# Kernel tuning notes

Measured on AMD Instinct MI355X. Metric: run time of the kernel, lower is better.

The kernel has to match this reference:

```python
import jax, jax.numpy as jnp
import numpy as np

B = 16384            # batch
F = 26               # number of categorical fields (columns of x)
FIELD_DIM = 100000   # vocab per field
D = 64               # base_embedding_dim
BLOCK_FIELDS = [list(range(0, 8)), list(range(8, 16)), list(range(16, 26))]
BLOCK_DIMS = [64, 32, 16]   # block 0 == base dim -> identity projector


def setup_inputs() -> dict:
    key = jax.random.key(0)
    ks = jax.random.split(key, 8)
    x = jax.random.randint(ks[0], (B, F), 0, FIELD_DIM, dtype=jnp.int32)
    # per-block embedding tables: rows = sum of field_dims of the block's fields
    t0 = jax.random.normal(ks[1], (len(BLOCK_FIELDS[0]) * FIELD_DIM, BLOCK_DIMS[0]), jnp.float32) * 0.02
    t1 = jax.random.normal(ks[2], (len(BLOCK_FIELDS[1]) * FIELD_DIM, BLOCK_DIMS[1]), jnp.float32) * 0.02
    t2 = jax.random.normal(ks[3], (len(BLOCK_FIELDS[2]) * FIELD_DIM, BLOCK_DIMS[2]), jnp.float32) * 0.02
    # projectors for blocks whose dim != base dim (torch Linear: y = x @ W.T + b)
    W1 = jax.random.normal(ks[4], (D, BLOCK_DIMS[1]), jnp.float32) * 0.05
    b1 = jnp.zeros((D,), jnp.float32)
    W2 = jax.random.normal(ks[5], (D, BLOCK_DIMS[2]), jnp.float32) * 0.05
    b2 = jnp.zeros((D,), jnp.float32)
    return {"x": x, "t0": t0, "t1": t1, "t2": t2, "W1": W1, "b1": b1, "W2": W2, "b2": b2}


def reference(x, t0, t1, t2, W1, b1, W2, b2):
    tables = [t0, t1, t2]
    projs = [None, (W1, b1), (W2, b2)]
    out = jnp.zeros((x.shape[0], D), dtype=t0.dtype)
    for blk in range(len(BLOCK_FIELDS)):
        fields = np.asarray(BLOCK_FIELDS[blk])                 # static column routing
        offs = jnp.arange(len(fields), dtype=x.dtype) * FIELD_DIM  # per-field row offsets
        idx = x[:, fields] + offs[None, :]                     # [B, nb]
        emb = tables[blk][idx]                                 # gather -> [B, nb, d_blk]
        if projs[blk] is not None:
            W, b = projs[blk]
            emb = jnp.einsum('bnd,od->bno', emb, W) + b        # project to base dim
        out = out + emb.sum(axis=1)                            # segment-sum over block's fields
    return out
```

## Files before the change

### kernel.cpp

```cpp
#include <hip/hip_runtime.h>
#include <hip/hip_bf16.h>

#define BATCH 16384
#define NFIELDS 26
#define FIELD_DIM 100000
#define BASED 64


__global__ __launch_bounds__(256) void mixdim_embbag_kernel(
    const int* __restrict__ x,
    const float* __restrict__ t0,
    const float* __restrict__ t1,
    const float* __restrict__ t2,
    const float* __restrict__ W1,
    const float* __restrict__ b1,
    const float* __restrict__ W2,
    const float* __restrict__ b2,
    float* __restrict__ out)
{
    const int lane = threadIdx.x & 63;
    const int wave = threadIdx.x >> 6;
    const int row  = blockIdx.x * 4 + wave;
    if (row >= BATCH) return;

    float w1r[32];
    {
        const float4* W1v = (const float4*)(W1 + lane * 32);
        #pragma unroll
        for (int i = 0; i < 8; ++i) {
            float4 v = W1v[i];
            w1r[4*i+0] = v.x; w1r[4*i+1] = v.y; w1r[4*i+2] = v.z; w1r[4*i+3] = v.w;
        }
    }
    float w2r[16];
    {
        const float4* W2v = (const float4*)(W2 + lane * 16);
        #pragma unroll
        for (int i = 0; i < 4; ++i) {
            float4 v = W2v[i];
            w2r[4*i+0] = v.x; w2r[4*i+1] = v.y; w2r[4*i+2] = v.z; w2r[4*i+3] = v.w;
        }
    }

    int xi = 0;
    if (lane < NFIELDS) xi = x[row * NFIELDS + lane];

    float acc = 0.f;
    #pragma unroll
    for (int f = 0; f < 8; ++f) {
        const int r = __shfl(xi, f) + f * FIELD_DIM;
        acc += t0[r * 64 + lane];
    }

    float s1 = 0.f;
    {
        const int d1 = lane & 31;
        #pragma unroll
        for (int f = 0; f < 8; ++f) {
            const int r = __shfl(xi, 8 + f) + f * FIELD_DIM;
            s1 += t1[r * 32 + d1];
        }
    }
    #pragma unroll
    for (int k = 0; k < 32; ++k)
        acc += __shfl(s1, k) * w1r[k];

    float s2 = 0.f;
    {
        const int d2 = lane & 15;
        #pragma unroll
        for (int f = 0; f < 10; ++f) {
            const int r = __shfl(xi, 16 + f) + f * FIELD_DIM;
            s2 += t2[r * 16 + d2];
        }
    }
    #pragma unroll
    for (int k = 0; k < 16; ++k)
        acc += __shfl(s2, k) * w2r[k];

    acc += 8.0f * b1[lane] + 10.0f * b2[lane];

    out[row * 64 + lane] = acc;
}

extern "C" void kernel_launch(void* const* d_in, const int* in_sizes, int n_in,
                              void* d_out, int out_size, void* d_ws, size_t ws_size,
                              hipStream_t stream) {
    const int*   x  = (const int*)  d_in[0];
    const float* t0 = (const float*)d_in[1];
    const float* t1 = (const float*)d_in[2];
    const float* t2 = (const float*)d_in[3];
    const float* W1 = (const float*)d_in[4];
    const float* b1 = (const float*)d_in[5];
    const float* W2 = (const float*)d_in[6];
    const float* b2 = (const float*)d_in[7];
    float* out = (float*)d_out;

    dim3 grid(BATCH / 4);
    dim3 block(256);
    hipLaunchKernelGGL(mixdim_embbag_kernel, grid, block, 0, stream,
                       x, t0, t1, t2, W1, b1, W2, b2, out);
}
```

Measured before the change: 329.3 us.

## Process two batch rows per wave with nontemporal table gathers

```diff
diff --git a/kernel.cpp b/kernel.cpp
--- a/kernel.cpp
+++ b/kernel.cpp
@@ -7,7 +7,11 @@
 #define BASED 64
 
 
-__global__ __launch_bounds__(256) void mixdim_embbag_kernel(
+__device__ __forceinline__ float ntload(const float* p) {
+    return __builtin_nontemporal_load(p);
+}
+
+__global__ __launch_bounds__(256, 4) void mixdim_embbag_kernel(
     const int* __restrict__ x,
     const float* __restrict__ t0,
     const float* __restrict__ t1,
@@ -20,8 +24,7 @@
 {
     const int lane = threadIdx.x & 63;
     const int wave = threadIdx.x >> 6;
-    const int row  = blockIdx.x * 4 + wave;
-    if (row >= BATCH) return;
+    const int row0 = (blockIdx.x * 4 + wave) * 2;
 
     float w1r[32];
     {
@@ -43,44 +46,65 @@
     }
 
     int xi = 0;
-    if (lane < NFIELDS) xi = x[row * NFIELDS + lane];
+    {
+        const int l = lane & 31;
+        const int r = row0 + (lane >> 5);
+        if (l < NFIELDS) xi = x[r * NFIELDS + l];
+    }
 
-    float acc = 0.f;
+    float acc0 = 0.f, acc1 = 0.f;
+
     #pragma unroll
     for (int f = 0; f < 8; ++f) {
-        const int r = __shfl(xi, f) + f * FIELD_DIM;
-        acc += t0[r * 64 + lane];
+        const int i0 = __shfl(xi, f)      + f * FIELD_DIM;
+        const int i1 = __shfl(xi, 32 + f) + f * FIELD_DIM;
+        acc0 += ntload(t0 + i0 * 64 + lane);
+        acc1 += ntload(t0 + i1 * 64 + lane);
     }
 
-    float s1 = 0.f;
+    float s1_0 = 0.f, s1_1 = 0.f;
     {
         const int d1 = lane & 31;
         #pragma unroll
-        for (int f = 0; f < 8; ++f) {
-            const int r = __shfl(xi, 8 + f) + f * FIELD_DIM;
-            s1 += t1[r * 32 + d1];
+        for (int j = 0; j < 8; ++j) {
+            const int i0 = __shfl(xi, 8 + j)      + j * FIELD_DIM;
+            const int i1 = __shfl(xi, 32 + 8 + j) + j * FIELD_DIM;
+            s1_0 += ntload(t1 + i0 * 32 + d1);
+            s1_1 += ntload(t1 + i1 * 32 + d1);
         }
     }
-    #pragma unroll
-    for (int k = 0; k < 32; ++k)
-        acc += __shfl(s1, k) * w1r[k];
 
-    float s2 = 0.f;
+    float s2_0 = 0.f, s2_1 = 0.f;
     {
         const int d2 = lane & 15;
         #pragma unroll
-        for (int f = 0; f < 10; ++f) {
-            const int r = __shfl(xi, 16 + f) + f * FIELD_DIM;
-            s2 += t2[r * 16 + d2];
+        for (int j = 0; j < 10; ++j) {
+            const int i0 = __shfl(xi, 16 + j)      + j * FIELD_DIM;
+            const int i1 = __shfl(xi, 32 + 16 + j) + j * FIELD_DIM;
+            s2_0 += ntload(t2 + i0 * 16 + d2);
+            s2_1 += ntload(t2 + i1 * 16 + d2);
         }
     }
+
     #pragma unroll
-    for (int k = 0; k < 16; ++k)
-        acc += __shfl(s2, k) * w2r[k];
+    for (int k = 0; k < 32; ++k) {
+        const float w = w1r[k];
+        acc0 += __shfl(s1_0, k) * w;
+        acc1 += __shfl(s1_1, k) * w;
+    }
+    #pragma unroll
+    for (int k = 0; k < 16; ++k) {
+        const float w = w2r[k];
+        acc0 += __shfl(s2_0, k) * w;
+        acc1 += __shfl(s2_1, k) * w;
+    }
 
-    acc += 8.0f * b1[lane] + 10.0f * b2[lane];
+    const float bias = 8.0f * b1[lane] + 10.0f * b2[lane];
+    acc0 += bias;
+    acc1 += bias;
 
-    out[row * 64 + lane] = acc;
+    out[row0 * 64 + lane]       = acc0;
+    out[(row0 + 1) * 64 + lane] = acc1;
 }
 
 extern "C" void kernel_launch(void* const* d_in, const int* in_sizes, int n_in,
@@ -96,7 +120,7 @@
     const float* b2 = (const float*)d_in[7];
     float* out = (float*)d_out;
 
-    dim3 grid(BATCH / 4);
+    dim3 grid(BATCH / 8);
     dim3 block(256);
     hipLaunchKernelGGL(mixdim_embbag_kernel, grid, block, 0, stream,
                        x, t0, t1, t2, W1, b1, W2, b2, out);
```

Measured after the change: 325.1 us. About the same (-1.3%).

## Process two rows per wave with vectorized nontemporal gathers and LDS projection

Applied to the files above, without the earlier changes.

```diff
diff --git a/kernel.cpp b/kernel.cpp
--- a/kernel.cpp
+++ b/kernel.cpp
@@ -4,10 +4,23 @@
 #define BATCH 16384
 #define NFIELDS 26
 #define FIELD_DIM 100000
-#define BASED 64
 
 
-__global__ __launch_bounds__(256) void mixdim_embbag_kernel(
+typedef float vf4 __attribute__((ext_vector_type(4)));
+
+__device__ __forceinline__ vf4 ntload4(const float* p) {
+    return __builtin_nontemporal_load((const vf4*)p);
+}
+__device__ __forceinline__ vf4 shflxor4(const vf4 v, int mask) {
+    vf4 r;
+    r.x = __shfl_xor(v.x, mask);
+    r.y = __shfl_xor(v.y, mask);
+    r.z = __shfl_xor(v.z, mask);
+    r.w = __shfl_xor(v.w, mask);
+    return r;
+}
+
+__global__ __launch_bounds__(256, 4) void mixdim_embbag_kernel(
     const int* __restrict__ x,
     const float* __restrict__ t0,
     const float* __restrict__ t1,
@@ -20,8 +33,17 @@
 {
     const int lane = threadIdx.x & 63;
     const int wave = threadIdx.x >> 6;
-    const int row  = blockIdx.x * 4 + wave;
-    if (row >= BATCH) return;
+    const int row0 = (blockIdx.x * 4 + wave) * 2;
+
+    __shared__ float lds[4 * 224];
+    float* wls = &lds[wave * 224];
+
+    int xi = 0;
+    {
+        const int l = lane & 31;
+        const int r = lane >> 5;
+        if (l < NFIELDS) xi = x[(row0 + r) * NFIELDS + l];
+    }
 
     float w1r[32];
     {
@@ -42,45 +64,92 @@
         }
     }
 
-    int xi = 0;
-    if (lane < NFIELDS) xi = x[row * NFIELDS + lane];
-
-    float acc = 0.f;
-    #pragma unroll
-    for (int f = 0; f < 8; ++f) {
-        const int r = __shfl(xi, f) + f * FIELD_DIM;
-        acc += t0[r * 64 + lane];
+    vf4 a0 = {0.f, 0.f, 0.f, 0.f};
+    {
+        const int c = lane & 15;
+        #pragma unroll
+        for (int g = 0; g < 4; ++g) {
+            const int P = g * 4 + (lane >> 4);
+            const int r = P & 1;
+            const int j = P >> 1;
+            const int idx = __shfl(xi, r * 32 + j) + j * FIELD_DIM;
+            a0 += ntload4(t0 + idx * 64 + c * 4);
+        }
+        a0 += shflxor4(a0, 32);
+        if (lane < 32) {
+            const int r = (lane >> 4) & 1;
+            *(vf4*)(wls + r * 64 + c * 4) = a0;
+        }
     }
 
-    float s1 = 0.f;
+    vf4 a1 = {0.f, 0.f, 0.f, 0.f};
     {
-        const int d1 = lane & 31;
+        const int c = lane & 7;
         #pragma unroll
-        for (int f = 0; f < 8; ++f) {
-            const int r = __shfl(xi, 8 + f) + f * FIELD_DIM;
-            s1 += t1[r * 32 + d1];
+        for (int g = 0; g < 2; ++g) {
+            const int P = g * 8 + (lane >> 3);
+            const int r = P & 1;
+            const int j = P >> 1;
+            const int idx = __shfl(xi, r * 32 + 8 + j) + j * FIELD_DIM;
+            a1 += ntload4(t1 + idx * 32 + c * 4);
+        }
+        a1 += shflxor4(a1, 16);
+        a1 += shflxor4(a1, 32);
+        if (lane < 16) {
+            const int r = (lane >> 3) & 1;
+            *(vf4*)(wls + 128 + r * 32 + c * 4) = a1;
         }
     }
-    #pragma unroll
-    for (int k = 0; k < 32; ++k)
-        acc += __shfl(s1, k) * w1r[k];
 
-    float s2 = 0.f;
+    vf4 a2 = {0.f, 0.f, 0.f, 0.f};
     {
-        const int d2 = lane & 15;
-        #pragma unroll
-        for (int f = 0; f < 10; ++f) {
-            const int r = __shfl(xi, 16 + f) + f * FIELD_DIM;
-            s2 += t2[r * 16 + d2];
+        const int c = lane & 3;
+        {
+            const int P = lane >> 2;
+            const int r = P & 1;
+            const int j = P >> 1;
+            const int idx = __shfl(xi, r * 32 + 16 + j) + j * FIELD_DIM;
+            a2 += ntload4(t2 + idx * 16 + c * 4);
+        }
+        {
+            const int P = 16 + (lane >> 2);
+            const int r = P & 1;
+            const int j = P >> 1;
+            const int idx = __shfl(xi, r * 32 + 16 + j) + j * FIELD_DIM;
+            if (P < 20)
+                a2 += ntload4(t2 + idx * 16 + c * 4);
+        }
+        a2 += shflxor4(a2, 8);
+        a2 += shflxor4(a2, 16);
+        a2 += shflxor4(a2, 32);
+        if (lane < 8) {
+            const int r = (lane >> 2) & 1;
+            *(vf4*)(wls + 192 + r * 16 + c * 4) = a2;
         }
     }
+
+    __syncthreads();
+
+    float acc0 = wls[0 + lane];
+    float acc1 = wls[64 + lane];
     #pragma unroll
-    for (int k = 0; k < 16; ++k)
-        acc += __shfl(s2, k) * w2r[k];
+    for (int k4 = 0; k4 < 8; ++k4) {
+        const float4 s0 = *(const float4*)(wls + 128 + k4 * 4);
+        const float4 s1 = *(const float4*)(wls + 160 + k4 * 4);
+        acc0 += s0.x * w1r[4*k4] + s0.y * w1r[4*k4+1] + s0.z * w1r[4*k4+2] + s0.w * w1r[4*k4+3];
+        acc1 += s1.x * w1r[4*k4] + s1.y * w1r[4*k4+1] + s1.z * w1r[4*k4+2] + s1.w * w1r[4*k4+3];
+    }
+    #pragma unroll
+    for (int k4 = 0; k4 < 4; ++k4) {
+        const float4 s0 = *(const float4*)(wls + 192 + k4 * 4);
+        const float4 s1 = *(const float4*)(wls + 208 + k4 * 4);
+        acc0 += s0.x * w2r[4*k4] + s0.y * w2r[4*k4+1] + s0.z * w2r[4*k4+2] + s0.w * w2r[4*k4+3];
+        acc1 += s1.x * w2r[4*k4] + s1.y * w2r[4*k4+1] + s1.z * w2r[4*k4+2] + s1.w * w2r[4*k4+3];
+    }
 
-    acc += 8.0f * b1[lane] + 10.0f * b2[lane];
-
-    out[row * 64 + lane] = acc;
+    const float bias = 8.0f * b1[lane] + 10.0f * b2[lane];
+    out[row0 * 64 + lane]       = acc0 + bias;
+    out[(row0 + 1) * 64 + lane] = acc1 + bias;
 }
 
 extern "C" void kernel_launch(void* const* d_in, const int* in_sizes, int n_in,
@@ -96,7 +165,7 @@
     const float* b2 = (const float*)d_in[7];
     float* out = (float*)d_out;
 
-    dim3 grid(BATCH / 4);
+    dim3 grid(BATCH / 8);
     dim3 block(256);
     hipLaunchKernelGGL(mixdim_embbag_kernel, grid, block, 0, stream,
                        x, t0, t1, t2, W1, b1, W2, b2, out);
```

After: 323.2 us. About the same (-1.9%).
